# Optimization experiments

Hardware: AMD Instinct MI355X
Metric: run time of the kernel (lower is better)

Reference implementation:

```python
import jax, jax.numpy as jnp
import numpy as np

B, S, E, H = 8, 1024, 1024, 16
EPS = 1e-3  # tf.keras LayerNormalization default epsilon


def setup_inputs() -> dict:
    key = jax.random.key(0)
    ks = jax.random.split(key, 5)
    x = jax.random.normal(ks[0], (B, S, E), dtype=jnp.float32)
    Wq = jax.random.normal(ks[1], (E, E), dtype=jnp.float32) * 0.02
    Wk = jax.random.normal(ks[2], (E, E), dtype=jnp.float32) * 0.02
    Wv = jax.random.normal(ks[3], (E, E), dtype=jnp.float32) * 0.02
    # original init is zeros; use small random values so the bias path is exercised
    rel_table = jax.random.normal(ks[4], (2 * S - 1, H), dtype=jnp.float32) * 0.02
    gamma = jnp.ones((E,), dtype=jnp.float32)
    beta = jnp.zeros((E,), dtype=jnp.float32)
    return {"x": x, "Wq": Wq, "Wk": Wk, "Wv": Wv, "rel_table": rel_table,
            "gamma": gamma, "beta": beta}


def reference(x, Wq, Wk, Wv, rel_table, gamma, beta):
    b, s, e = x.shape
    h = rel_table.shape[1]
    scale = e ** (-0.5)  # NOTE: scales by full emb_size, not head_dim (faithful)

    def split_heads(t):  # (b, s, e) -> (b, h, s, d)
        return t.reshape(b, s, h, -1).transpose(0, 2, 1, 3)

    q = split_heads(x @ Wq)
    k = split_heads(x @ Wk)
    v = split_heads(x @ Wv)

    attn = jnp.einsum("bhqd,bhkd->bhqk", q, k) * scale
    attn = jax.nn.softmax(attn, axis=-1)

    # relative bias: gather then the exact (quirky) reshape sequence of the original
    r = jnp.arange(s)
    rel_index = jnp.clip(r[None, :] - r[:, None] + (s - 1), 0, 2 * s - 2)  # (s, s)
    bias = rel_table[rel_index]              # (s, s, h)
    bias = bias.reshape(-1).reshape(h, s, s)  # faithful flat-order reinterpretation
    attn = attn + bias[None]  # added POST-softmax, as in the original

    out = jnp.einsum("bhqk,bhkd->bhqd", attn, v)
    out = out.transpose(0, 2, 1, 3).reshape(b, s, e)

    # LayerNorm over last axis
    mu = jnp.mean(out, axis=-1, keepdims=True)
    var = jnp.var(out, axis=-1, keepdims=True)
    out = (out - mu) / jnp.sqrt(var + EPS) * gamma + beta
    return out
```

## Files before the change

### kernel.cpp

```cpp
#include <hip/hip_runtime.h>
#include <hip/hip_bf16.h>

#define PB 8
#define PS 1024
#define PE 1024
#define PH 16
#define PD 64
#define EPSLN 1e-3f
#define SCALE 0.03125f

typedef __attribute__((ext_vector_type(8))) short bf16x8;
typedef __attribute__((ext_vector_type(4))) float f32x4;
typedef __attribute__((ext_vector_type(16))) float f32x16;

__device__ __forceinline__ unsigned short f2bf(float f) {
    unsigned int u = __float_as_uint(f);
    u += 0x7FFFu + ((u >> 16) & 1u);
    return (unsigned short)(u >> 16);
}

__device__ __forceinline__ void gload_lds16(const void* g, void* l) {
    __builtin_amdgcn_global_load_lds(
        (const __attribute__((address_space(1))) unsigned int*)g,
        (__attribute__((address_space(3))) unsigned int*)l,
        16, 0, 0);
}

__device__ __forceinline__ unsigned int cvtpk_bf16(float lo, float hi) {
    unsigned int r;
    asm("v_cvt_pk_bf16_f32 %0, %1, %2" : "=v"(r) : "v"(lo), "v"(hi));
    return r;
}

__device__ __forceinline__ void plswap(unsigned int& a, unsigned int& b) {
    asm("v_permlane32_swap_b32 %0, %1" : "+v"(a), "+v"(b));
}

#define SWZF(row, chunk) (((chunk) ^ ((row) & 7) ^ (((row) >> 3) & 3)))

__global__ __launch_bounds__(256) void conv_x(
    const float* __restrict__ X, unsigned short* __restrict__ Xb)
{
    const size_t i = (size_t)blockIdx.x * 256 + threadIdx.x;
    const float4* p = reinterpret_cast<const float4*>(X) + i * 2;
    float4 a = p[0], b = p[1];
    unsigned short r[8];
    r[0] = f2bf(a.x); r[1] = f2bf(a.y); r[2] = f2bf(a.z); r[3] = f2bf(a.w);
    r[4] = f2bf(b.x); r[5] = f2bf(b.y); r[6] = f2bf(b.z); r[7] = f2bf(b.w);
    *reinterpret_cast<uint4*>(Xb + i * 8) = *reinterpret_cast<const uint4*>(r);
}

__global__ __launch_bounds__(256) void conv_w(
    const float* __restrict__ Wq, const float* __restrict__ Wk,
    const float* __restrict__ Wv, unsigned short* __restrict__ Wtb)
{
    const int proj = blockIdx.z;
    const float* W = (proj == 0) ? Wq : (proj == 1) ? Wk : Wv;
    __shared__ float tile[32][33];
    const int n0 = blockIdx.x * 32, k0 = blockIdx.y * 32;
    const int tx = threadIdx.x & 31, ty = threadIdx.x >> 5;
#pragma unroll
    for (int i = 0; i < 4; ++i)
        tile[ty + i * 8][tx] = W[(size_t)(k0 + ty + i * 8) * PE + n0 + tx];
    __syncthreads();
#pragma unroll
    for (int i = 0; i < 4; ++i)
        Wtb[(size_t)(proj * 1024 + n0 + ty + i * 8) * 1024 + k0 + tx] =
            f2bf(tile[tx][ty + i * 8]);
}

__global__ __launch_bounds__(256) void conv_rel(
    const float* __restrict__ rel, unsigned short* __restrict__ relbf)
{
    const int i = blockIdx.x * 1024 + threadIdx.x * 4;
#pragma unroll
    for (int k = 0; k < 4; ++k)
        if (i + k < (2 * PS - 1) * PH) relbf[i + k] = f2bf(rel[i + k]);
}

__global__ __launch_bounds__(256) void qkv_mfma(
    const unsigned short* __restrict__ Xb,
    const unsigned short* __restrict__ Wtb,
    unsigned short* __restrict__ QKV)
{
    const int orig = blockIdx.x;
    const int wg = (orig & 7) * 192 + (orig >> 3);
    const int nblk = wg % 24, mblk = wg / 24;
    const int m0 = mblk * 128, n0 = nblk * 128;

    __shared__ __align__(16) unsigned short As[128 * 64];
    __shared__ __align__(16) unsigned short Bs[128 * 64];

    const int t = threadIdx.x;
    const int w = t >> 6, l = t & 63;
    const int lane15 = l & 15, lhi = l >> 4;
    const int wm = w >> 1, wn = w & 1;

    f32x4 acc[4][4] = {};

    for (int k0 = 0; k0 < 1024; k0 += 64) {
        __syncthreads();
#pragma unroll
        for (int c = 0; c < 4; ++c) {
            const int ci = (w * 4 + c) * 64 + l;
            const int r = ci >> 3;
            const int srccl = (ci & 7) ^ (r & 7);
            gload_lds16(Xb  + (size_t)(m0 + r) * 1024 + k0 + srccl * 8, &As[ci * 8]);
            gload_lds16(Wtb + (size_t)(n0 + r) * 1024 + k0 + srccl * 8, &Bs[ci * 8]);
        }
        __syncthreads();
#pragma unroll
        for (int kk = 0; kk < 2; ++kk) {
            bf16x8 af[4], bf[4];
#pragma unroll
            for (int mi = 0; mi < 4; ++mi) {
                const int row = wm * 64 + mi * 16 + lane15;
                af[mi] = *reinterpret_cast<const bf16x8*>(
                    &As[row * 64 + (((kk * 4 + lhi) ^ (row & 7)) << 3)]);
            }
#pragma unroll
            for (int ni = 0; ni < 4; ++ni) {
                const int row = wn * 64 + ni * 16 + lane15;
                bf[ni] = *reinterpret_cast<const bf16x8*>(
                    &Bs[row * 64 + (((kk * 4 + lhi) ^ (row & 7)) << 3)]);
            }
#pragma unroll
            for (int mi = 0; mi < 4; ++mi)
#pragma unroll
                for (int ni = 0; ni < 4; ++ni)
                    acc[mi][ni] = __builtin_amdgcn_mfma_f32_16x16x32_bf16(
                        af[mi], bf[ni], acc[mi][ni], 0, 0, 0);
        }
    }
#pragma unroll
    for (int mi = 0; mi < 4; ++mi)
#pragma unroll
        for (int ni = 0; ni < 4; ++ni)
#pragma unroll
            for (int r = 0; r < 4; ++r) {
                const int gr = m0 + wm * 64 + mi * 16 + lhi * 4 + r;
                const int gc = n0 + wn * 64 + ni * 16 + lane15;
                QKV[(size_t)gr * 3072 + gc] = f2bf(acc[mi][ni][r]);
            }
}

__global__ __launch_bounds__(256) void vtrans(
    const unsigned short* __restrict__ QKV, unsigned short* __restrict__ VT)
{
    const int j0 = blockIdx.x * 64, b = blockIdx.y, h = blockIdx.z;
    __shared__ unsigned short tile[64][72];
    const int t = threadIdx.x;

#pragma unroll
    for (int it = 0; it < 2; ++it) {
        const int jr = it * 32 + (t >> 3), dc = t & 7;
        uint4 d = *reinterpret_cast<const uint4*>(
            QKV + ((size_t)(b * PS + j0 + jr)) * 3072 + 2048 + h * 64 + dc * 8);
        *reinterpret_cast<uint4*>(&tile[jr][dc * 8]) = d;
    }
    __syncthreads();
    const int d = t & 63, jc = t >> 6;
    unsigned short out[16];
#pragma unroll
    for (int k = 0; k < 16; ++k) out[k] = tile[jc * 16 + k][d];
    unsigned short* dst = VT + ((size_t)((h * 8 + b) * 64 + d)) * 1024 + j0 + jc * 16;
    *reinterpret_cast<uint4*>(dst)     = *reinterpret_cast<const uint4*>(out);
    *reinterpret_cast<uint4*>(dst + 8) = *reinterpret_cast<const uint4*>(out + 8);
}

__global__ __launch_bounds__(256) void attn_mfma(
    const unsigned short* __restrict__ qkv,
    const unsigned short* __restrict__ VT,
    const unsigned short* __restrict__ relbf,
    float* __restrict__ O)
{
    __shared__ __align__(16) unsigned short Ks[2][64 * 64];
    __shared__ __align__(16) unsigned short Vt[2][64 * 64];

    const int orig = blockIdx.x;
    const int wg = (orig & 7) * 128 + (orig >> 3);
    const int qt = wg & 7;
    const int h  = (wg >> 3) & 15;
    const int b  = wg >> 7;

    const int t = threadIdx.x;
    const int w = t >> 6, l = t & 63;
    const int lane31 = l & 31, hi = l >> 5;

    const int qrow_g = qt * 128 + w * 32 + lane31;

    bf16x8 qf[4];
    {
        const unsigned short* qp =
            qkv + ((size_t)(b * PS) + qrow_g) * 3072 + h * 64 + hi * 8;
#pragma unroll
        for (int dw = 0; dw < 4; ++dw)
            qf[dw] = *reinterpret_cast<const bf16x8*>(qp + dw * 16);
    }

    const unsigned short* Kg = qkv + (size_t)(b * PS) * 3072 + 1024 + h * 64;
    const unsigned short* Vg = VT + ((size_t)((h * 8 + b) * 64)) * 1024;

    const int s1 = (h << 6) | (qrow_g >> 4);
    const int s2hi = (qrow_g & 15) << 6;
    const unsigned short* relp = relbf + (size_t)(s2hi - s1 + PS - 1) * PH + hi * 8;

    f32x16 accP[2] = {};
    f32x16 accB[2] = {};
    f32x16 accL = {};
    bf16x8 ones;
#pragma unroll
    for (int i = 0; i < 8; ++i) ones[i] = (short)0x3F80;

#define ATTN_STAGE(buf, j0)                                                          \
    {                                                                                \
        _Pragma("unroll")                                                            \
        for (int it = 0; it < 2; ++it) {                                             \
            const int ci = it * 256 + t;                                             \
            const int r = ci >> 3;                                                   \
            const int scl = SWZF(r, ci & 7);                                         \
            gload_lds16(Kg + (size_t)((j0) + r) * 3072 + scl * 8, &Ks[buf][ci * 8]); \
            gload_lds16(Vg + (size_t)r * 1024 + (j0) + scl * 8, &Vt[buf][ci * 8]);   \
        }                                                                            \
    }

    ATTN_STAGE(0, 0)

    for (int tt = 0; tt < 16; ++tt) {
        const int cur = tt & 1;
        const int j0 = tt * 64;

        bf16x8 af[4];
        __builtin_amdgcn_sched_barrier(0);
#pragma unroll
        for (int jw = 0; jw < 4; ++jw)
            af[jw] = *reinterpret_cast<const bf16x8*>(relp + j0 + jw * 16);
        __builtin_amdgcn_sched_barrier(0);
        if (tt < 15) {
            ATTN_STAGE(cur ^ 1, j0 + 64)
            __builtin_amdgcn_sched_barrier(0);
            asm volatile("s_waitcnt vmcnt(8)" ::: "memory");
        } else {
            asm volatile("s_waitcnt vmcnt(4)" ::: "memory");
        }
        __builtin_amdgcn_sched_barrier(0);
        __builtin_amdgcn_s_barrier();
        __builtin_amdgcn_sched_barrier(0);

        bf16x8 pfrag[4];
#pragma unroll
        for (int jt = 0; jt < 2; ++jt) {
            f32x16 sc = {};
            __builtin_amdgcn_s_setprio(1);
#pragma unroll
            for (int dw = 0; dw < 4; ++dw) {
                const int row = jt * 32 + lane31;
                bf16x8 aK = *reinterpret_cast<const bf16x8*>(
                    &Ks[cur][row * 64 + (SWZF(row, dw * 2 + hi) << 3)]);
                sc = __builtin_amdgcn_mfma_f32_32x32x16_bf16(aK, qf[dw], sc, 0, 0, 0);
            }
            __builtin_amdgcn_s_setprio(0);
            float p[16];
#pragma unroll
            for (int r = 0; r < 16; ++r) p[r] = __expf(sc[r] * SCALE);
            unsigned int a0 = cvtpk_bf16(p[0],  p[1]),  a1 = cvtpk_bf16(p[2],  p[3]);
            unsigned int b0 = cvtpk_bf16(p[4],  p[5]),  b1 = cvtpk_bf16(p[6],  p[7]);
            unsigned int c0 = cvtpk_bf16(p[8],  p[9]),  c1 = cvtpk_bf16(p[10], p[11]);
            unsigned int d0 = cvtpk_bf16(p[12], p[13]), d1 = cvtpk_bf16(p[14], p[15]);
            plswap(a0, b0); plswap(a1, b1);
            plswap(c0, d0); plswap(c1, d1);
            union { unsigned int u[4]; bf16x8 v; } pk0, pk1;
            pk0.u[0] = a0; pk0.u[1] = a1; pk0.u[2] = b0; pk0.u[3] = b1;
            pk1.u[0] = c0; pk1.u[1] = c1; pk1.u[2] = d0; pk1.u[3] = d1;
            pfrag[jt * 2]     = pk0.v;
            pfrag[jt * 2 + 1] = pk1.v;
        }

        __builtin_amdgcn_s_setprio(1);
#pragma unroll
        for (int jw = 0; jw < 4; ++jw) {
            accL = __builtin_amdgcn_mfma_f32_32x32x16_bf16(pfrag[jw], ones, accL, 0, 0, 0);
#pragma unroll
            for (int dt = 0; dt < 2; ++dt) {
                const int row = dt * 32 + lane31;
                bf16x8 bV = *reinterpret_cast<const bf16x8*>(
                    &Vt[cur][row * 64 + (SWZF(row, jw * 2 + hi) << 3)]);
                accP[dt] = __builtin_amdgcn_mfma_f32_32x32x16_bf16(
                    pfrag[jw], bV, accP[dt], 0, 0, 0);
                accB[dt] = __builtin_amdgcn_mfma_f32_32x32x16_bf16(
                    af[jw], bV, accB[dt], 0, 0, 0);
            }
        }
        __builtin_amdgcn_s_setprio(0);
        __builtin_amdgcn_s_barrier();
    }
#undef ATTN_STAGE

#pragma unroll
    for (int dt = 0; dt < 2; ++dt)
#pragma unroll
        for (int r = 0; r < 16; ++r) {
            const int rl = (r & 3) + 8 * (r >> 2) + 4 * hi;
            O[((size_t)(b * PS + qt * 128 + w * 32 + rl)) * PE + h * 64 + dt * 32 + lane31]
                = accP[dt][r] / accL[r] + accB[dt][r];
        }
}

__global__ __launch_bounds__(256) void layernorm_inplace(
    float* __restrict__ O,
    const float* __restrict__ gamma,
    const float* __restrict__ beta)
{
    const int row = blockIdx.x;
    float* p = O + (size_t)row * PE;
    const int t = threadIdx.x;

    float4 x = reinterpret_cast<float4*>(p)[t];
    float s  = x.x + x.y + x.z + x.w;
    float s2 = x.x * x.x + x.y * x.y + x.z * x.z + x.w * x.w;

#pragma unroll
    for (int off = 1; off < 64; off <<= 1) {
        s  += __shfl_xor(s, off, 64);
        s2 += __shfl_xor(s2, off, 64);
    }
    __shared__ float red[2][4];
    const int wid = t >> 6;
    if ((t & 63) == 0) { red[0][wid] = s; red[1][wid] = s2; }
    __syncthreads();
    const float ts  = red[0][0] + red[0][1] + red[0][2] + red[0][3];
    const float ts2 = red[1][0] + red[1][1] + red[1][2] + red[1][3];

    const float mu  = ts * (1.f / PE);
    const float var = ts2 * (1.f / PE) - mu * mu;
    const float inv = rsqrtf(var + EPSLN);

    const float4 g  = reinterpret_cast<const float4*>(gamma)[t];
    const float4 bb = reinterpret_cast<const float4*>(beta)[t];
    float4 y;
    y.x = (x.x - mu) * inv * g.x + bb.x;
    y.y = (x.y - mu) * inv * g.y + bb.y;
    y.z = (x.z - mu) * inv * g.z + bb.z;
    y.w = (x.w - mu) * inv * g.w + bb.w;
    reinterpret_cast<float4*>(p)[t] = y;
}

extern "C" void kernel_launch(void* const* d_in, const int* in_sizes, int n_in,
                              void* d_out, int out_size, void* d_ws, size_t ws_size,
                              hipStream_t stream) {
    (void)in_sizes; (void)n_in; (void)out_size; (void)ws_size;
    const float* x     = (const float*)d_in[0];
    const float* Wq    = (const float*)d_in[1];
    const float* Wk    = (const float*)d_in[2];
    const float* Wv    = (const float*)d_in[3];
    const float* rel   = (const float*)d_in[4];
    const float* gamma = (const float*)d_in[5];
    const float* beta  = (const float*)d_in[6];
    float* out = (float*)d_out;

    char* ws = (char*)d_ws;
    unsigned short* Xb    = (unsigned short*)ws;
    unsigned short* Wtb   = (unsigned short*)(ws + 16777216);
    unsigned short* QKV   = (unsigned short*)(ws + 23068672);
    unsigned short* VT    = (unsigned short*)(ws + 73400320);
    unsigned short* relbf = (unsigned short*)ws;

    conv_x<<<4096, 256, 0, stream>>>(x, Xb);
    conv_w<<<dim3(32, 32, 3), 256, 0, stream>>>(Wq, Wk, Wv, Wtb);
    qkv_mfma<<<1536, 256, 0, stream>>>(Xb, Wtb, QKV);
    conv_rel<<<32, 256, 0, stream>>>(rel, relbf);
    vtrans<<<dim3(16, 8, 16), 256, 0, stream>>>(QKV, VT);
    attn_mfma<<<1024, 256, 0, stream>>>(QKV, VT, relbf, out);
    layernorm_inplace<<<PB * PS, 256, 0, stream>>>(out, gamma, beta);
}
```

Baseline: 171.3 us.

## Restructure QKV GEMM to 256x256 tiles with double-buffered LDS pipeline

New measurement: 211.9 us. 1.24x slower.

```diff
diff --git a/kernel.cpp b/kernel.cpp
--- a/kernel.cpp
+++ b/kernel.cpp
@@ -78,67 +78,156 @@
         if (i + k < (2 * PS - 1) * PH) relbf[i + k] = f2bf(rel[i + k]);
 }
 
-__global__ __launch_bounds__(256) void qkv_mfma(
+__global__ __launch_bounds__(512, 2) void qkv_mfma(
     const unsigned short* __restrict__ Xb,
     const unsigned short* __restrict__ Wtb,
     unsigned short* __restrict__ QKV)
 {
     const int orig = blockIdx.x;
-    const int wg = (orig & 7) * 192 + (orig >> 3);
-    const int nblk = wg % 24, mblk = wg / 24;
-    const int m0 = mblk * 128, n0 = nblk * 128;
-
-    __shared__ __align__(16) unsigned short As[128 * 64];
-    __shared__ __align__(16) unsigned short Bs[128 * 64];
+    const int wg = (orig & 7) * 48 + (orig >> 3);
+    const int nblk = wg % 12, mblk = wg / 12;
+    const int m0 = mblk * 256, n0 = nblk * 256;
+
+    __shared__ __align__(16) unsigned short As[2][256 * 64];
+    __shared__ __align__(16) unsigned short Bs[2][256 * 64];
 
     const int t = threadIdx.x;
-    const int w = t >> 6, l = t & 63;
+    const int l = t & 63, w = t >> 6;
     const int lane15 = l & 15, lhi = l >> 4;
-    const int wm = w >> 1, wn = w & 1;
-
-    f32x4 acc[4][4] = {};
-
-    for (int k0 = 0; k0 < 1024; k0 += 64) {
-        __syncthreads();
-#pragma unroll
-        for (int c = 0; c < 4; ++c) {
-            const int ci = (w * 4 + c) * 64 + l;
-            const int r = ci >> 3;
-            const int srccl = (ci & 7) ^ (r & 7);
-            gload_lds16(Xb  + (size_t)(m0 + r) * 1024 + k0 + srccl * 8, &As[ci * 8]);
-            gload_lds16(Wtb + (size_t)(n0 + r) * 1024 + k0 + srccl * 8, &Bs[ci * 8]);
-        }
-        __syncthreads();
-#pragma unroll
-        for (int kk = 0; kk < 2; ++kk) {
-            bf16x8 af[4], bf[4];
-#pragma unroll
-            for (int mi = 0; mi < 4; ++mi) {
-                const int row = wm * 64 + mi * 16 + lane15;
-                af[mi] = *reinterpret_cast<const bf16x8*>(
-                    &As[row * 64 + (((kk * 4 + lhi) ^ (row & 7)) << 3)]);
-            }
-#pragma unroll
-            for (int ni = 0; ni < 4; ++ni) {
+    const int wm = w >> 2, wn = w & 3;
+
+    f32x4 acc[8][4] = {};
+
+#define QSTAGE_A(kt, c)                                                         \
+    {                                                                           \
+        _Pragma("unroll")                                                       \
+        for (int rr = 0; rr < 4; ++rr) {                                        \
+            const int ci = rr * 512 + t;                                        \
+            const int r = ci >> 3;                                              \
+            const int scl = SWZF(r, ci & 7);                                    \
+            gload_lds16(Xb + (size_t)(m0 + r) * 1024 + (kt) * 64 + scl * 8,     \
+                        &As[c][ci * 8]);                                        \
+        }                                                                       \
+    }
+#define QSTAGE_B(kt, c)                                                         \
+    {                                                                           \
+        _Pragma("unroll")                                                       \
+        for (int rr = 0; rr < 4; ++rr) {                                        \
+            const int ci = rr * 512 + t;                                        \
+            const int r = ci >> 3;                                              \
+            const int scl = SWZF(r, ci & 7);                                    \
+            gload_lds16(Wtb + (size_t)(n0 + r) * 1024 + (kt) * 64 + scl * 8,    \
+                        &Bs[c][ci * 8]);                                        \
+        }                                                                       \
+    }
+
+    QSTAGE_A(0, 0) QSTAGE_B(0, 0)
+    QSTAGE_A(1, 1) QSTAGE_B(1, 1)
+
+    for (int kt = 0; kt < 16; ++kt) {
+        const int c = kt & 1;
+        if (kt < 14) { asm volatile("s_waitcnt vmcnt(8)" ::: "memory"); }
+        else         { asm volatile("s_waitcnt vmcnt(0)" ::: "memory"); }
+        __builtin_amdgcn_sched_barrier(0);
+        __builtin_amdgcn_s_barrier();
+        __builtin_amdgcn_sched_barrier(0);
+
+        bf16x8 af[8][2], bf[4][2];
+#pragma unroll
+        for (int mi = 0; mi < 4; ++mi)
+#pragma unroll
+            for (int kk = 0; kk < 2; ++kk) {
+                const int row = wm * 128 + mi * 16 + lane15;
+                af[mi][kk] = *reinterpret_cast<const bf16x8*>(
+                    &As[c][row * 64 + (SWZF(row, kk * 4 + lhi) << 3)]);
+            }
+#pragma unroll
+        for (int ni = 0; ni < 2; ++ni)
+#pragma unroll
+            for (int kk = 0; kk < 2; ++kk) {
                 const int row = wn * 64 + ni * 16 + lane15;
-                bf[ni] = *reinterpret_cast<const bf16x8*>(
-                    &Bs[row * 64 + (((kk * 4 + lhi) ^ (row & 7)) << 3)]);
-            }
-#pragma unroll
-            for (int mi = 0; mi < 4; ++mi)
-#pragma unroll
-                for (int ni = 0; ni < 4; ++ni)
+                bf[ni][kk] = *reinterpret_cast<const bf16x8*>(
+                    &Bs[c][row * 64 + (SWZF(row, kk * 4 + lhi) << 3)]);
+            }
+        asm volatile("s_waitcnt lgkmcnt(0)" ::: "memory");
+        __builtin_amdgcn_sched_barrier(0);
+        __builtin_amdgcn_s_setprio(1);
+#pragma unroll
+        for (int mi = 0; mi < 4; ++mi)
+#pragma unroll
+            for (int ni = 0; ni < 2; ++ni)
+#pragma unroll
+                for (int kk = 0; kk < 2; ++kk)
                     acc[mi][ni] = __builtin_amdgcn_mfma_f32_16x16x32_bf16(
-                        af[mi], bf[ni], acc[mi][ni], 0, 0, 0);
-        }
-    }
-#pragma unroll
-    for (int mi = 0; mi < 4; ++mi)
+                        af[mi][kk], bf[ni][kk], acc[mi][ni], 0, 0, 0);
+        __builtin_amdgcn_s_setprio(0);
+
+#pragma unroll
+        for (int mi = 4; mi < 8; ++mi)
+#pragma unroll
+            for (int kk = 0; kk < 2; ++kk) {
+                const int row = wm * 128 + mi * 16 + lane15;
+                af[mi][kk] = *reinterpret_cast<const bf16x8*>(
+                    &As[c][row * 64 + (SWZF(row, kk * 4 + lhi) << 3)]);
+            }
+#pragma unroll
+        for (int ni = 2; ni < 4; ++ni)
+#pragma unroll
+            for (int kk = 0; kk < 2; ++kk) {
+                const int row = wn * 64 + ni * 16 + lane15;
+                bf[ni][kk] = *reinterpret_cast<const bf16x8*>(
+                    &Bs[c][row * 64 + (SWZF(row, kk * 4 + lhi) << 3)]);
+            }
+        asm volatile("s_waitcnt lgkmcnt(0)" ::: "memory");
+        __builtin_amdgcn_sched_barrier(0);
+        __builtin_amdgcn_s_setprio(1);
+#pragma unroll
+        for (int mi = 0; mi < 4; ++mi)
+#pragma unroll
+            for (int ni = 2; ni < 4; ++ni)
+#pragma unroll
+                for (int kk = 0; kk < 2; ++kk)
+                    acc[mi][ni] = __builtin_amdgcn_mfma_f32_16x16x32_bf16(
+                        af[mi][kk], bf[ni][kk], acc[mi][ni], 0, 0, 0);
+        __builtin_amdgcn_s_setprio(0);
+        __builtin_amdgcn_sched_barrier(0);
+        __builtin_amdgcn_s_barrier();
+        __builtin_amdgcn_sched_barrier(0);
+
+        if (kt < 14) { QSTAGE_A(kt + 2, c) }
+        __builtin_amdgcn_s_setprio(1);
+#pragma unroll
+        for (int mi = 4; mi < 8; ++mi)
+#pragma unroll
+            for (int ni = 0; ni < 2; ++ni)
+#pragma unroll
+                for (int kk = 0; kk < 2; ++kk)
+                    acc[mi][ni] = __builtin_amdgcn_mfma_f32_16x16x32_bf16(
+                        af[mi][kk], bf[ni][kk], acc[mi][ni], 0, 0, 0);
+        __builtin_amdgcn_s_setprio(0);
+
+        if (kt < 14) { QSTAGE_B(kt + 2, c) }
+        __builtin_amdgcn_s_setprio(1);
+#pragma unroll
+        for (int mi = 4; mi < 8; ++mi)
+#pragma unroll
+            for (int ni = 2; ni < 4; ++ni)
+#pragma unroll
+                for (int kk = 0; kk < 2; ++kk)
+                    acc[mi][ni] = __builtin_amdgcn_mfma_f32_16x16x32_bf16(
+                        af[mi][kk], bf[ni][kk], acc[mi][ni], 0, 0, 0);
+        __builtin_amdgcn_s_setprio(0);
+    }
+#undef QSTAGE_A
+#undef QSTAGE_B
+
+#pragma unroll
+    for (int mi = 0; mi < 8; ++mi)
 #pragma unroll
         for (int ni = 0; ni < 4; ++ni)
 #pragma unroll
             for (int r = 0; r < 4; ++r) {
-                const int gr = m0 + wm * 64 + mi * 16 + lhi * 4 + r;
+                const int gr = m0 + wm * 128 + mi * 16 + lhi * 4 + r;
                 const int gc = n0 + wn * 64 + ni * 16 + lane15;
                 QKV[(size_t)gr * 3072 + gc] = f2bf(acc[mi][ni][r]);
             }
@@ -367,7 +456,7 @@
 
     conv_x<<<4096, 256, 0, stream>>>(x, Xb);
     conv_w<<<dim3(32, 32, 3), 256, 0, stream>>>(Wq, Wk, Wv, Wtb);
-    qkv_mfma<<<1536, 256, 0, stream>>>(Xb, Wtb, QKV);
+    qkv_mfma<<<384, 512, 0, stream>>>(Xb, Wtb, QKV);
     conv_rel<<<32, 256, 0, stream>>>(rel, relbf);
     vtrans<<<dim3(16, 8, 16), 256, 0, stream>>>(QKV, VT);
     attn_mfma<<<1024, 256, 0, stream>>>(QKV, VT, relbf, out);
```
